# Optimization experiments

Measured on AMD Instinct MI355X. Metric: run time of the kernel, lower is better.

Reference implementation:

```python
import jax, jax.numpy as jnp
import numpy as np

S, D, H, DK, DV = 4096, 1024, 16, 64, 64


def setup_inputs() -> dict:
    key = jax.random.key(0)
    ks = jax.random.split(key, 6)
    x = jax.random.normal(ks[0], (S, D), dtype=jnp.float32)
    # per-head projection weights, stacked over heads; scaled for numerical sanity
    Wq = jax.random.normal(ks[1], (H, D, DK), dtype=jnp.float32) / np.sqrt(D)
    Wk = jax.random.normal(ks[2], (H, D, DK), dtype=jnp.float32) / np.sqrt(D)
    Wv = jax.random.normal(ks[3], (H, D, DV), dtype=jnp.float32) / np.sqrt(D)
    Wc = jax.random.normal(ks[4], (H * DV, D), dtype=jnp.float32) / np.sqrt(H * DV)
    bc = jnp.zeros((D,), dtype=jnp.float32)
    return {"x": x, "Wq": Wq, "Wk": Wk, "Wv": Wv, "Wc": Wc, "bc": bc}


def reference(x, Wq, Wk, Wv, Wc, bc):
    # Per-head projections (original loops over heads with separate Linears;
    # stacking over h is the same math, vectorized).
    q = jnp.einsum("sd,hdk->hsk", x, Wq)   # [H,S,DK]
    k = jnp.einsum("sd,hdk->hsk", x, Wk)   # [H,S,DK]
    v = jnp.einsum("sd,hdv->hsv", x, Wv)   # [H,S,DV]
    scores = jnp.einsum("hsk,htk->hst", q, k) / jnp.sqrt(jnp.asarray(DK, x.dtype))
    probs = jax.nn.softmax(scores, axis=-1)  # softmax over last dim, per row
    o = jnp.einsum("hst,htv->hsv", probs, v)  # [H,S,DV]
    cat = jnp.transpose(o, (1, 0, 2)).reshape(S, H * DV)  # concat heads on last dim
    return cat @ Wc + bc  # output projection with bias
```

## Files before the change

kernel.cpp:

```cpp
#include <hip/hip_runtime.h>
#include <hip/hip_bf16.h>

#define S_ 4096
#define D_ 1024
#define H_ 16
#define DK_ 64
#define DV_ 64

typedef short bf16x8 __attribute__((ext_vector_type(8)));
typedef short bf16x4 __attribute__((ext_vector_type(4)));
typedef float floatx4 __attribute__((ext_vector_type(4)));
using bf16 = __hip_bfloat16;

#define MFMA16(a, b, c) __builtin_amdgcn_mfma_f32_16x16x32_bf16(a, b, c, 0, 0, 0)

#if __has_builtin(__builtin_amdgcn_exp2f)
#define EXP2(x) __builtin_amdgcn_exp2f(x)
#else
#define EXP2(x) exp2f(x)
#endif

__device__ __forceinline__ void stage16(const void* g, void* l) {
    __builtin_amdgcn_global_load_lds(
        (const __attribute__((address_space(1))) void*)g,
        (__attribute__((address_space(3))) void*)l, 16, 0, 0);
}

__device__ __forceinline__ bf16x8 ldsfrag(const bf16* base, int row, int chunk) {
    return *(const bf16x8*)(base + row * 64 + (((chunk ^ (row & 7))) << 3));
}
__device__ __forceinline__ bf16x8 ldsfrag32(const bf16* base, int row, int chunk) {
    return *(const bf16x8*)(base + row * 32 + (((chunk ^ (row & 3))) << 3));
}

__device__ __forceinline__ unsigned short bfbits(float f) {
    union { bf16 h; unsigned short u; } c; c.h = __float2bfloat16(f); return c.u;
}
__device__ __forceinline__ float bf2f(bf16 h) { return __bfloat162float(h); }
__device__ __forceinline__ unsigned int pkrne(float lo, float hi) {
    return (unsigned int)bfbits(lo) | ((unsigned int)bfbits(hi) << 16);
}

__device__ __forceinline__ unsigned int pktrunc(float lo, float hi) {
    union { float f; unsigned int u; } a, b;
    a.f = hi; b.f = lo;
    return __builtin_amdgcn_perm(a.u, b.u, 0x07060302u);
}

__global__ __launch_bounds__(256)
void prep(const float* __restrict__ x, const float* __restrict__ Wq,
          const float* __restrict__ Wk, const float* __restrict__ Wv,
          const float* __restrict__ Wc,
          bf16* __restrict__ xb, bf16* __restrict__ Wt, bf16* __restrict__ Wct)
{
    __shared__ float ls[64][65];
    const int bx = blockIdx.x, t = threadIdx.x;

    if (bx < 2048) {
        int i = bx * 2048 + t * 8;
        float4 a = *(const float4*)(x + i);
        float4 b = *(const float4*)(x + i + 4);
        ushort4 lo, hi;
        lo.x = bfbits(a.x); lo.y = bfbits(a.y); lo.z = bfbits(a.z); lo.w = bfbits(a.w);
        hi.x = bfbits(b.x); hi.y = bfbits(b.y); hi.z = bfbits(b.z); hi.w = bfbits(b.w);
        *(ushort4*)(xb + i) = lo;
        *(ushort4*)(xb + i + 4) = hi;
        return;
    }
    if (bx < 2816) {
        const int idx = bx - 2048;
        const int z = idx >> 4, which = z >> 4, h = z & 15;
        const float* s = (which == 0 ? Wq : which == 1 ? Wk : Wv) + (size_t)h * D_ * 64;
        bf16* d = Wt + ((size_t)which * 1024 + h * 64) * D_;
        const float scale = (which == 0) ? 0.125f * 1.44269504088896340736f : 1.0f;
        const int r0 = (idx & 15) * 64;
        {
            int r = t >> 2, cseg = (t & 3) * 16;
            const float* sp = s + (size_t)(r0 + r) * 64 + cseg;
            #pragma unroll
            for (int i = 0; i < 16; i += 4) {
                float4 v = *(const float4*)(sp + i);
                ls[r][cseg + i + 0] = v.x; ls[r][cseg + i + 1] = v.y;
                ls[r][cseg + i + 2] = v.z; ls[r][cseg + i + 3] = v.w;
            }
        }
        __syncthreads();
        {
            int c = t >> 2, rseg = (t & 3) * 16;
            bf16* dp = d + (size_t)c * D_ + r0 + rseg;
            #pragma unroll
            for (int i = 0; i < 16; i++) dp[i] = __float2bfloat16(ls[rseg + i][c] * scale);
        }
        return;
    }
    {
        const int idx = bx - 2816;
        const int r0 = (idx & 15) * 64, c0 = (idx >> 4) * 64;
        {
            int r = t >> 2, cseg = (t & 3) * 16;
            const float* sp = Wc + (size_t)(r0 + r) * D_ + c0 + cseg;
            #pragma unroll
            for (int i = 0; i < 16; i += 4) {
                float4 v = *(const float4*)(sp + i);
                ls[r][cseg + i + 0] = v.x; ls[r][cseg + i + 1] = v.y;
                ls[r][cseg + i + 2] = v.z; ls[r][cseg + i + 3] = v.w;
            }
        }
        __syncthreads();
        {
            int c = t >> 2, rseg = (t & 3) * 16;
            bf16* dp = Wct + (size_t)(c0 + c) * D_ + r0 + rseg;
            #pragma unroll
            for (int i = 0; i < 16; i++) dp[i] = __float2bfloat16(ls[rseg + i][c]);
        }
    }
}

__global__ __launch_bounds__(256)
void qkv_gemm(const bf16* __restrict__ xb, const bf16* __restrict__ Wt,
              bf16* __restrict__ Qb, bf16* __restrict__ Kb, bf16* __restrict__ Vtb)
{
    const int m0 = blockIdx.x * 128;
    const int n0 = blockIdx.y * 128;
    __shared__ __align__(16) bf16 xa[2][128 * 32];
    __shared__ __align__(16) bf16 wb2[2][128 * 32];

    const int t = threadIdx.x, lane = t & 63, w = t >> 6;
    const int l15 = lane & 15, quad = lane >> 4;

    auto stage_a = [&](int buf, int kk) {
        #pragma unroll
        for (int j = 0; j < 2; j++) {
            int row = j * 64 + (t >> 2);
            int ch  = (t & 3) ^ (row & 3);
            stage16((const char*)xb + ((size_t)(m0 + row) * D_ + kk) * 2 + ch * 16,
                    (char*)&xa[buf][0] + (j * 4 + w) * 1024);
        }
    };
    auto stage_b = [&](int buf, int kk) {
        #pragma unroll
        for (int j = 0; j < 2; j++) {
            int row = j * 64 + (t >> 2);
            int ch  = (t & 3) ^ (row & 3);
            stage16((const char*)Wt + ((size_t)(n0 + row) * D_ + kk) * 2 + ch * 16,
                    (char*)&wb2[buf][0] + (j * 4 + w) * 1024);
        }
    };

    const floatx4 fz = {0.f, 0.f, 0.f, 0.f};
    floatx4 acc[2][8];
    #pragma unroll
    for (int mt = 0; mt < 2; mt++)
        #pragma unroll
        for (int nt = 0; nt < 8; nt++) acc[mt][nt] = fz;

    const int which = n0 >> 10;

    stage_a(0, 0); stage_b(0, 0);
    if (which != 2) {
        for (int kt = 0; kt < 32; kt++) {
            int cur = kt & 1;
            __syncthreads();
            if (kt < 31) { stage_a(cur ^ 1, (kt + 1) * 32); stage_b(cur ^ 1, (kt + 1) * 32); }
            bf16x8 a0 = ldsfrag32(&xa[cur][0], w * 32 + l15,      quad);
            bf16x8 a1 = ldsfrag32(&xa[cur][0], w * 32 + 16 + l15, quad);
            #pragma unroll
            for (int nt = 0; nt < 8; nt++) {
                bf16x8 b = ldsfrag32(&wb2[cur][0], nt * 16 + l15, quad);
                acc[0][nt] = MFMA16(b, a0, acc[0][nt]);
                acc[1][nt] = MFMA16(b, a1, acc[1][nt]);
            }
        }
        bf16* base = (which == 0) ? Qb : Kb;
        #pragma unroll
        for (int nt = 0; nt < 8; nt++) {
            int n  = n0 + nt * 16 + quad * 4;
            int hh = (n >> 6) & 15, col = n & 63;
            #pragma unroll
            for (int mt = 0; mt < 2; mt++) {
                int s = m0 + w * 32 + mt * 16 + l15;
                uint2 o;
                o.x = pkrne(acc[mt][nt][0], acc[mt][nt][1]);
                o.y = pkrne(acc[mt][nt][2], acc[mt][nt][3]);
                *(uint2*)(base + ((size_t)hh * S_ + s) * 64 + col) = o;
            }
        }
    } else {
        for (int kt = 0; kt < 32; kt++) {
            int cur = kt & 1;
            __syncthreads();
            if (kt < 31) { stage_a(cur ^ 1, (kt + 1) * 32); stage_b(cur ^ 1, (kt + 1) * 32); }
            bf16x8 a0 = ldsfrag32(&xa[cur][0], w * 32 + l15,      quad);
            bf16x8 a1 = ldsfrag32(&xa[cur][0], w * 32 + 16 + l15, quad);
            #pragma unroll
            for (int nt = 0; nt < 8; nt++) {
                bf16x8 b = ldsfrag32(&wb2[cur][0], nt * 16 + l15, quad);
                acc[0][nt] = MFMA16(a0, b, acc[0][nt]);
                acc[1][nt] = MFMA16(a1, b, acc[1][nt]);
            }
        }
        #pragma unroll
        for (int nt = 0; nt < 8; nt++) {
            int n = n0 + nt * 16 + l15;
            int hh = (n >> 6) & 15, col = n & 63;
            #pragma unroll
            for (int mt = 0; mt < 2; mt++) {
                int s = m0 + w * 32 + mt * 16 + quad * 4;
                uint2 o;
                o.x = pkrne(acc[mt][nt][0], acc[mt][nt][1]);
                o.y = pkrne(acc[mt][nt][2], acc[mt][nt][3]);
                *(uint2*)(Vtb + ((size_t)hh * 64 + col) * S_ + s) = o;
            }
        }
    }
}

template<int NKT, bool FULL>
__global__ __attribute__((amdgpu_waves_per_eu(4, 4))) __launch_bounds__(256)
void attn(const bf16* __restrict__ Qb, const bf16* __restrict__ Kb,
          const bf16* __restrict__ Vtb, bf16* __restrict__ Cat,
          bf16* __restrict__ Opart, float* __restrict__ lpart)
{
    const int m0 = blockIdx.x * 128;
    const int h  = blockIdx.y;
    const int half = blockIdx.z;
    const int keybase = half * (NKT * 64);

    __shared__ __align__(16) bf16 ka[2][64 * 64];
    __shared__ __align__(16) bf16 vt[2][64 * 64];

    const int t = threadIdx.x, lane = t & 63, w = t >> 6;
    const int l15 = lane & 15, quad = lane >> 4;

    auto stage_kv = [&](int buf, int key0) {
        const char* kg = (const char*)(Kb + ((size_t)h * S_ + key0) * 64);
        #pragma unroll
        for (int j = 0; j < 2; j++) {
            int c = (j * 4 + w) * 64 + lane;
            int row = c >> 3, ch = (c & 7) ^ (row & 7);
            stage16(kg + row * 128 + ch * 16, (char*)&ka[buf][0] + (j * 4 + w) * 1024);
        }
        const char* vg = (const char*)(Vtb + (size_t)h * 64 * S_ + key0);
        #pragma unroll
        for (int j = 0; j < 2; j++) {
            int c = (j * 4 + w) * 64 + lane;
            int row = c >> 3, ch = (c & 7) ^ (row & 7);
            stage16(vg + (size_t)row * (S_ * 2) + ch * 16, (char*)&vt[buf][0] + (j * 4 + w) * 1024);
        }
    };

    bf16x8 qf[2][2];
    #pragma unroll
    for (int nq = 0; nq < 2; nq++)
        #pragma unroll
        for (int ks = 0; ks < 2; ks++)
            qf[nq][ks] = *(const bf16x8*)(Qb +
                ((size_t)h * S_ + m0 + w * 32 + nq * 16 + l15) * 64 + ks * 32 + quad * 8);

    const floatx4 fz = {0.f, 0.f, 0.f, 0.f};
    floatx4 acc[2][4];
    float rs[2] = {0.f, 0.f};
    #pragma unroll
    for (int nq = 0; nq < 2; nq++)
        #pragma unroll
        for (int nt = 0; nt < 4; nt++) acc[nq][nt] = fz;

    stage_kv(0, keybase);
    __syncthreads();

    for (int kt = 0; kt < NKT; kt++) {
        const int cur = kt & 1;
        if (kt + 1 < NKT) stage_kv(cur ^ 1, keybase + (kt + 1) * 64);

        floatx4 sc[4][2];
        #pragma unroll
        for (int mk = 0; mk < 4; mk++)
            #pragma unroll
            for (int nq = 0; nq < 2; nq++) sc[mk][nq] = fz;
        #pragma unroll
        for (int ks = 0; ks < 2; ks++) {
            bf16x8 af[4];
            #pragma unroll
            for (int mk = 0; mk < 4; mk++)
                af[mk] = ldsfrag(&ka[cur][0], mk * 16 + l15, ks * 4 + quad);
            #pragma unroll
            for (int mk = 0; mk < 4; mk++)
                #pragma unroll
                for (int nq = 0; nq < 2; nq++)
                    sc[mk][nq] = MFMA16(af[mk], qf[nq][ks], sc[mk][nq]);
        }

        union bf4u { bf16x4 v; unsigned int u[2]; };
        bf4u pf[4][2];
        #pragma unroll
        for (int mk = 0; mk < 4; mk++)
            #pragma unroll
            for (int nq = 0; nq < 2; nq++) {
                float p0 = EXP2(sc[mk][nq][0]);
                float p1 = EXP2(sc[mk][nq][1]);
                float p2 = EXP2(sc[mk][nq][2]);
                float p3 = EXP2(sc[mk][nq][3]);
                rs[nq] += (p0 + p1) + (p2 + p3);
                pf[mk][nq].u[0] = pktrunc(p0, p1);
                pf[mk][nq].u[1] = pktrunc(p2, p3);
            }

        #pragma unroll
        for (int p = 0; p < 2; p++) {
            union { bf16x8 v8; bf16x4 v4[2]; } b8[2];
            #pragma unroll
            for (int nq = 0; nq < 2; nq++) {
                b8[nq].v4[0] = pf[2 * p + 0][nq].v;
                b8[nq].v4[1] = pf[2 * p + 1][nq].v;
            }
            #pragma unroll
            for (int nt = 0; nt < 4; nt++) {
                const char* vb = (const char*)&vt[cur][0]
                               + (nt * 16 + l15) * 128 + (quad & 1) * 8;
                const int r7 = l15 & 7;
                union { bf16x8 v8; bf16x4 v4[2]; } a8;
                a8.v4[0] = *(const bf16x4*)(vb + (((4 * p +     (quad >> 1)) ^ r7) << 4));
                a8.v4[1] = *(const bf16x4*)(vb + (((4 * p + 2 + (quad >> 1)) ^ r7) << 4));
                #pragma unroll
                for (int nq = 0; nq < 2; nq++)
                    acc[nq][nt] = MFMA16(a8.v8, b8[nq].v8, acc[nq][nt]);
            }
        }
        __syncthreads();
    }

    #pragma unroll
    for (int nq = 0; nq < 2; nq++) {
        rs[nq] += __shfl_xor(rs[nq], 16);
        rs[nq] += __shfl_xor(rs[nq], 32);
    }

    if (FULL) {
        #pragma unroll
        for (int nq = 0; nq < 2; nq++) {
            float inv = 1.0f / rs[nq];
            int q = m0 + w * 32 + nq * 16 + l15;
            #pragma unroll
            for (int nt = 0; nt < 4; nt++) {
                uint2 o;
                o.x = pktrunc(acc[nq][nt][0] * inv, acc[nq][nt][1] * inv);
                o.y = pktrunc(acc[nq][nt][2] * inv, acc[nq][nt][3] * inv);
                *(uint2*)(Cat + (size_t)q * (H_ * DV_) + h * 64 + nt * 16 + quad * 4) = o;
            }
        }
    } else {
        const size_t plane = (size_t)(half * H_ + h) * S_;
        #pragma unroll
        for (int nq = 0; nq < 2; nq++) {
            int q = m0 + w * 32 + nq * 16 + l15;
            #pragma unroll
            for (int nt = 0; nt < 4; nt++) {
                uint2 o;
                o.x = pktrunc(acc[nq][nt][0], acc[nq][nt][1]);
                o.y = pktrunc(acc[nq][nt][2], acc[nq][nt][3]);
                *(uint2*)(Opart + (plane + q) * 64 + nt * 16 + quad * 4) = o;
            }
            if (quad == 0) lpart[plane + q] = rs[nq];
        }
    }
}

__global__ __launch_bounds__(256)
void combine(const bf16* __restrict__ Opart, const float* __restrict__ lpart,
             bf16* __restrict__ Cat)
{
    const int h = blockIdx.y;
    const int off = (blockIdx.x * 256 + threadIdx.x) * 8;
    const int s = off >> 6, dv = off & 63;
    union { bf16x8 v; bf16 e[8]; } o0, o1;
    o0.v = *(const bf16x8*)(Opart + (size_t)h * S_ * 64 + off);
    o1.v = *(const bf16x8*)(Opart + (size_t)(H_ + h) * S_ * 64 + off);
    float inv = 1.0f / (lpart[(size_t)h * S_ + s] + lpart[(size_t)(H_ + h) * S_ + s]);
    uint4 o;
    o.x = pktrunc((bf2f(o0.e[0]) + bf2f(o1.e[0])) * inv, (bf2f(o0.e[1]) + bf2f(o1.e[1])) * inv);
    o.y = pktrunc((bf2f(o0.e[2]) + bf2f(o1.e[2])) * inv, (bf2f(o0.e[3]) + bf2f(o1.e[3])) * inv);
    o.z = pktrunc((bf2f(o0.e[4]) + bf2f(o1.e[4])) * inv, (bf2f(o0.e[5]) + bf2f(o1.e[5])) * inv);
    o.w = pktrunc((bf2f(o0.e[6]) + bf2f(o1.e[6])) * inv, (bf2f(o0.e[7]) + bf2f(o1.e[7])) * inv);
    *(uint4*)(Cat + (size_t)s * (H_ * DV_) + h * 64 + dv) = o;
}

__global__ __launch_bounds__(256)
void out_proj(const bf16* __restrict__ Cat, const bf16* __restrict__ Wct,
              const float* __restrict__ bc, float* __restrict__ out)
{
    const int m0 = blockIdx.x * 128;
    const int n0 = blockIdx.y * 64;
    __shared__ __align__(16) bf16 ca[2][128 * 32];
    __shared__ __align__(16) bf16 wb2[2][64 * 32];

    const int t = threadIdx.x, lane = t & 63, w = t >> 6;
    const int l15 = lane & 15, quad = lane >> 4;

    auto stage_a = [&](int buf, int kk) {
        #pragma unroll
        for (int j = 0; j < 2; j++) {
            int row = j * 64 + (t >> 2);
            int ch  = (t & 3) ^ (row & 3);
            stage16((const char*)Cat + ((size_t)(m0 + row) * D_ + kk) * 2 + ch * 16,
                    (char*)&ca[buf][0] + (j * 4 + w) * 1024);
        }
    };
    auto stage_b = [&](int buf, int kk) {
        int row = t >> 2;
        int ch  = (t & 3) ^ (row & 3);
        stage16((const char*)Wct + ((size_t)(n0 + row) * D_ + kk) * 2 + ch * 16,
                (char*)&wb2[buf][0] + w * 1024);
    };

    const floatx4 fz = {0.f, 0.f, 0.f, 0.f};
    floatx4 acc[2][4];
    #pragma unroll
    for (int mt = 0; mt < 2; mt++)
        #pragma unroll
        for (int nt = 0; nt < 4; nt++) acc[mt][nt] = fz;

    stage_a(0, 0); stage_b(0, 0);
    for (int kt = 0; kt < 32; kt++) {
        int cur = kt & 1;
        __syncthreads();
        if (kt < 31) { stage_a(cur ^ 1, (kt + 1) * 32); stage_b(cur ^ 1, (kt + 1) * 32); }
        bf16x8 a0 = ldsfrag32(&ca[cur][0], w * 32 + l15,      quad);
        bf16x8 a1 = ldsfrag32(&ca[cur][0], w * 32 + 16 + l15, quad);
        #pragma unroll
        for (int nt = 0; nt < 4; nt++) {
            bf16x8 b = ldsfrag32(&wb2[cur][0], nt * 16 + l15, quad);
            acc[0][nt] = MFMA16(a0, b, acc[0][nt]);
            acc[1][nt] = MFMA16(a1, b, acc[1][nt]);
        }
    }

    #pragma unroll
    for (int nt = 0; nt < 4; nt++) {
        int col = n0 + nt * 16 + l15;
        float bias = bc[col];
        #pragma unroll
        for (int mt = 0; mt < 2; mt++)
            #pragma unroll
            for (int r = 0; r < 4; r++) {
                int row = m0 + w * 32 + mt * 16 + quad * 4 + r;
                out[(size_t)row * D_ + col] = acc[mt][nt][r] + bias;
            }
    }
}

extern "C" void kernel_launch(void* const* d_in, const int* in_sizes, int n_in,
                              void* d_out, int out_size, void* d_ws, size_t ws_size,
                              hipStream_t stream)
{
    const float* x  = (const float*)d_in[0];
    const float* Wq = (const float*)d_in[1];
    const float* Wk = (const float*)d_in[2];
    const float* Wv = (const float*)d_in[3];
    const float* Wc = (const float*)d_in[4];
    const float* bc = (const float*)d_in[5];
    float* out = (float*)d_out;

    bf16* xb  = (bf16*)d_ws;
    bf16* Cat = xb;
    bf16* Wt  = xb  + (size_t)S_ * D_;
    bf16* Wct = Wt  + (size_t)3 * H_ * 64 * D_;
    bf16* Qb  = Wct + (size_t)D_ * H_ * DV_;
    bf16* Kb  = Qb  + (size_t)H_ * S_ * 64;
    bf16* Vtb = Kb  + (size_t)H_ * S_ * 64;
    bf16* Opart = Vtb + (size_t)H_ * 64 * S_;
    float* lpart = (float*)(Opart + (size_t)2 * H_ * S_ * 64);

    const size_t need_split = (size_t)((char*)(lpart + (size_t)2 * H_ * S_) - (char*)d_ws);
    const bool split = ws_size >= need_split;

    prep<<<dim3(3072), 256, 0, stream>>>(x, Wq, Wk, Wv, Wc, xb, Wt, Wct);
    qkv_gemm<<<dim3(S_ / 128, 3072 / 128), 256, 0, stream>>>(xb, Wt, Qb, Kb, Vtb);

    if (split) {
        attn<32, false><<<dim3(S_ / 128, H_, 2), 256, 0, stream>>>(
            Qb, Kb, Vtb, Cat, Opart, lpart);
        combine<<<dim3(S_ * 64 / 2048, H_), 256, 0, stream>>>(Opart, lpart, Cat);
    } else {
        attn<64, true><<<dim3(S_ / 128, H_, 1), 256, 0, stream>>>(
            Qb, Kb, Vtb, Cat, Opart, lpart);
    }

    out_proj<<<dim3(S_ / 128, D_ / 64), 256, 0, stream>>>(Cat, Wct, bc, out);
}
```

Baseline: 238.1 us.

## Double query tile per attention block and compute row sums with MFMA

Each attention block now handles 256 query rows instead of 128, with each wave covering 64 rows, so every staged K/V tile is reused across twice as many queries. The softmax row sums are now accumulated by an MFMA against a vector of bf16 ones on the truncated probabilities, replacing the scalar adds and cross-lane shuffles. The occupancy hint drops to 2 waves per EU to make room for the larger accumulator set. In exchange the grid has half as many blocks, register pressure rises, and the row sums now come from bf16-rounded probabilities.

```diff
diff --git a/kernel.cpp b/kernel.cpp
--- a/kernel.cpp
+++ b/kernel.cpp
@@ -216,12 +216,12 @@
 }
 
 template<int NKT, bool FULL>
-__global__ __attribute__((amdgpu_waves_per_eu(4, 4))) __launch_bounds__(256)
+__global__ __attribute__((amdgpu_waves_per_eu(2))) __launch_bounds__(256)
 void attn(const bf16* __restrict__ Qb, const bf16* __restrict__ Kb,
           const bf16* __restrict__ Vtb, bf16* __restrict__ Cat,
           bf16* __restrict__ Opart, float* __restrict__ lpart)
 {
-    const int m0 = blockIdx.x * 128;
+    const int m0 = blockIdx.x * 256;
     const int h  = blockIdx.y;
     const int half = blockIdx.z;
     const int keybase = half * (NKT * 64);
@@ -249,21 +249,27 @@
         }
     };
 
-    bf16x8 qf[2][2];
-    #pragma unroll
-    for (int nq = 0; nq < 2; nq++)
+    bf16x8 qf[4][2];
+    #pragma unroll
+    for (int nq = 0; nq < 4; nq++)
         #pragma unroll
         for (int ks = 0; ks < 2; ks++)
             qf[nq][ks] = *(const bf16x8*)(Qb +
-                ((size_t)h * S_ + m0 + w * 32 + nq * 16 + l15) * 64 + ks * 32 + quad * 8);
+                ((size_t)h * S_ + m0 + w * 64 + nq * 16 + l15) * 64 + ks * 32 + quad * 8);
+
+    bf16x8 ones8;
+    #pragma unroll
+    for (int i = 0; i < 8; i++) ones8[i] = (short)0x3F80;
 
     const floatx4 fz = {0.f, 0.f, 0.f, 0.f};
-    floatx4 acc[2][4];
-    float rs[2] = {0.f, 0.f};
-    #pragma unroll
-    for (int nq = 0; nq < 2; nq++)
+    floatx4 acc[4][4];
+    floatx4 rsa[4];
+    #pragma unroll
+    for (int nq = 0; nq < 4; nq++) {
+        rsa[nq] = fz;
         #pragma unroll
         for (int nt = 0; nt < 4; nt++) acc[nq][nt] = fz;
+    }
 
     stage_kv(0, keybase);
     __syncthreads();
@@ -272,47 +278,41 @@
         const int cur = kt & 1;
         if (kt + 1 < NKT) stage_kv(cur ^ 1, keybase + (kt + 1) * 64);
 
-        floatx4 sc[4][2];
-        #pragma unroll
-        for (int mk = 0; mk < 4; mk++)
-            #pragma unroll
-            for (int nq = 0; nq < 2; nq++) sc[mk][nq] = fz;
-        #pragma unroll
-        for (int ks = 0; ks < 2; ks++) {
-            bf16x8 af[4];
-            #pragma unroll
-            for (int mk = 0; mk < 4; mk++)
-                af[mk] = ldsfrag(&ka[cur][0], mk * 16 + l15, ks * 4 + quad);
-            #pragma unroll
-            for (int mk = 0; mk < 4; mk++)
-                #pragma unroll
-                for (int nq = 0; nq < 2; nq++)
-                    sc[mk][nq] = MFMA16(af[mk], qf[nq][ks], sc[mk][nq]);
-        }
-
         union bf4u { bf16x4 v; unsigned int u[2]; };
-        bf4u pf[4][2];
-        #pragma unroll
-        for (int mk = 0; mk < 4; mk++)
-            #pragma unroll
-            for (int nq = 0; nq < 2; nq++) {
-                float p0 = EXP2(sc[mk][nq][0]);
-                float p1 = EXP2(sc[mk][nq][1]);
-                float p2 = EXP2(sc[mk][nq][2]);
-                float p3 = EXP2(sc[mk][nq][3]);
-                rs[nq] += (p0 + p1) + (p2 + p3);
+        bf4u pf[4][4];
+        #pragma unroll
+        for (int mk = 0; mk < 4; mk++) {
+            bf16x8 a0 = ldsfrag(&ka[cur][0], mk * 16 + l15, quad);
+            bf16x8 a1 = ldsfrag(&ka[cur][0], mk * 16 + l15, 4 + quad);
+            floatx4 s[4];
+            #pragma unroll
+            for (int nq = 0; nq < 4; nq++) s[nq] = fz;
+            #pragma unroll
+            for (int nq = 0; nq < 4; nq++) s[nq] = MFMA16(a0, qf[nq][0], s[nq]);
+            #pragma unroll
+            for (int nq = 0; nq < 4; nq++) s[nq] = MFMA16(a1, qf[nq][1], s[nq]);
+            #pragma unroll
+            for (int nq = 0; nq < 4; nq++) {
+                float p0 = EXP2(s[nq][0]);
+                float p1 = EXP2(s[nq][1]);
+                float p2 = EXP2(s[nq][2]);
+                float p3 = EXP2(s[nq][3]);
                 pf[mk][nq].u[0] = pktrunc(p0, p1);
                 pf[mk][nq].u[1] = pktrunc(p2, p3);
             }
+        }
 
         #pragma unroll
         for (int p = 0; p < 2; p++) {
-            union { bf16x8 v8; bf16x4 v4[2]; } b8[2];
-            #pragma unroll
-            for (int nq = 0; nq < 2; nq++) {
+            union { bf16x8 v8; bf16x4 v4[2]; } b8[4];
+            #pragma unroll
+            for (int nq = 0; nq < 4; nq++) {
                 b8[nq].v4[0] = pf[2 * p + 0][nq].v;
                 b8[nq].v4[1] = pf[2 * p + 1][nq].v;
             }
+            #pragma unroll
+            for (int nq = 0; nq < 4; nq++)
+                rsa[nq] = MFMA16(ones8, b8[nq].v8, rsa[nq]);
             #pragma unroll
             for (int nt = 0; nt < 4; nt++) {
                 const char* vb = (const char*)&vt[cur][0]
@@ -322,24 +322,18 @@
                 a8.v4[0] = *(const bf16x4*)(vb + (((4 * p +     (quad >> 1)) ^ r7) << 4));
                 a8.v4[1] = *(const bf16x4*)(vb + (((4 * p + 2 + (quad >> 1)) ^ r7) << 4));
                 #pragma unroll
-                for (int nq = 0; nq < 2; nq++)
+                for (int nq = 0; nq < 4; nq++)
                     acc[nq][nt] = MFMA16(a8.v8, b8[nq].v8, acc[nq][nt]);
             }
         }
         __syncthreads();
     }
 
-    #pragma unroll
-    for (int nq = 0; nq < 2; nq++) {
-        rs[nq] += __shfl_xor(rs[nq], 16);
-        rs[nq] += __shfl_xor(rs[nq], 32);
-    }
-
     if (FULL) {
         #pragma unroll
-        for (int nq = 0; nq < 2; nq++) {
-            float inv = 1.0f / rs[nq];
-            int q = m0 + w * 32 + nq * 16 + l15;
+        for (int nq = 0; nq < 4; nq++) {
+            float inv = 1.0f / rsa[nq][0];
+            int q = m0 + w * 64 + nq * 16 + l15;
             #pragma unroll
             for (int nt = 0; nt < 4; nt++) {
                 uint2 o;
@@ -351,8 +345,8 @@
     } else {
         const size_t plane = (size_t)(half * H_ + h) * S_;
         #pragma unroll
-        for (int nq = 0; nq < 2; nq++) {
-            int q = m0 + w * 32 + nq * 16 + l15;
+        for (int nq = 0; nq < 4; nq++) {
+            int q = m0 + w * 64 + nq * 16 + l15;
             #pragma unroll
             for (int nt = 0; nt < 4; nt++) {
                 uint2 o;
@@ -360,7 +354,7 @@
                 o.y = pktrunc(acc[nq][nt][2], acc[nq][nt][3]);
                 *(uint2*)(Opart + (plane + q) * 64 + nt * 16 + quad * 4) = o;
             }
-            if (quad == 0) lpart[plane + q] = rs[nq];
+            if (quad == 0) lpart[plane + q] = rsa[nq][0];
         }
     }
 }
@@ -477,11 +471,11 @@
     qkv_gemm<<<dim3(S_ / 128, 3072 / 128), 256, 0, stream>>>(xb, Wt, Qb, Kb, Vtb);
 
     if (split) {
-        attn<32, false><<<dim3(S_ / 128, H_, 2), 256, 0, stream>>>(
+        attn<32, false><<<dim3(S_ / 256, H_, 2), 256, 0, stream>>>(
             Qb, Kb, Vtb, Cat, Opart, lpart);
         combine<<<dim3(S_ * 64 / 2048, H_), 256, 0, stream>>>(Opart, lpart, Cat);
     } else {
-        attn<64, true><<<dim3(S_ / 128, H_, 1), 256, 0, stream>>>(
+        attn<64, true><<<dim3(S_ / 256, H_, 1), 256, 0, stream>>>(
             Qb, Kb, Vtb, Cat, Opart, lpart);
     }
 
```

After: 231.8 us. -2.6%, faster.
